# Kernel tuning notes

Measured on AMD Instinct MI355X. Metric: run time of the kernel, lower is better.

Reference implementation:

```python
import jax, jax.numpy as jnp
import numpy as np

N, E, F_IN, H, C, G, NC = 50000, 800000, 128, 4, 64, 512, 10
NEG_SLOPE = 0.2


def setup_inputs() -> dict:
    key = jax.random.key(0)
    ks = jax.random.split(key, 16)
    s = lambda fan: 1.0 / np.sqrt(fan)
    inp = {
        'x': jax.random.normal(ks[0], (N, F_IN), jnp.float32),
        'edge_index': jax.random.randint(ks[1], (2, E), 0, N, jnp.int64),
        'batch': jnp.sort(jax.random.randint(ks[2], (N,), 0, G, jnp.int64)),
        # conv1: F_IN -> H*C, concat
        'W1': jax.random.normal(ks[3], (F_IN, H * C), jnp.float32) * s(F_IN),
        'a_src1': jax.random.normal(ks[4], (H, C), jnp.float32) * s(C),
        'a_dst1': jax.random.normal(ks[5], (H, C), jnp.float32) * s(C),
        'b1': jnp.zeros((H * C,), jnp.float32),
        # conv2: H*C -> H*C, concat
        'W2': jax.random.normal(ks[6], (H * C, H * C), jnp.float32) * s(H * C),
        'a_src2': jax.random.normal(ks[7], (H, C), jnp.float32) * s(C),
        'a_dst2': jax.random.normal(ks[8], (H, C), jnp.float32) * s(C),
        'b2': jnp.zeros((H * C,), jnp.float32),
        # conv3: H*C -> C, concat=False (mean over heads)
        'W3': jax.random.normal(ks[9], (H * C, H * C), jnp.float32) * s(H * C),
        'a_src3': jax.random.normal(ks[10], (H, C), jnp.float32) * s(C),
        'a_dst3': jax.random.normal(ks[11], (H, C), jnp.float32) * s(C),
        'b3': jnp.zeros((C,), jnp.float32),
        # final linear: C -> NC
        'Wl': jax.random.normal(ks[12], (C, NC), jnp.float32) * s(C),
        'bl': jnp.zeros((NC,), jnp.float32),
    }
    return inp


def _gat_conv(x, src, dst, W, a_src, a_dst, b, concat):
    n = x.shape[0]
    h = (x @ W).reshape(n, H, C)                       # [N,H,C]
    al_src = jnp.sum(h * a_src, axis=-1)               # [N,H]
    al_dst = jnp.sum(h * a_dst, axis=-1)               # [N,H]
    e = al_src[src] + al_dst[dst]                      # [E',H] per-edge logits
    e = jax.nn.leaky_relu(e, NEG_SLOPE)
    # segment softmax over incoming edges of each dst node
    m = jax.ops.segment_max(e, dst, num_segments=n)
    ex = jnp.exp(e - m[dst])
    z = jax.ops.segment_sum(ex, dst, num_segments=n)
    alpha = ex / (z[dst] + 1e-16)                      # [E',H]
    msg = h[src] * alpha[:, :, None]                   # [E',H,C]
    out = jax.ops.segment_sum(msg, dst, num_segments=n)  # [N,H,C]
    out = out.reshape(n, H * C) if concat else out.mean(axis=1)
    return out + b


def reference(x, edge_index, batch, W1, a_src1, a_dst1, b1, W2, a_src2, a_dst2, b2,
              W3, a_src3, a_dst3, b3, Wl, bl):
    n = x.shape[0]
    loops = jnp.arange(n, dtype=edge_index.dtype)
    src = jnp.concatenate([edge_index[0], loops])      # add self-loops (PyG default)
    dst = jnp.concatenate([edge_index[1], loops])
    h = jax.nn.relu(_gat_conv(x, src, dst, W1, a_src1, a_dst1, b1, True))
    h = jax.nn.relu(_gat_conv(h, src, dst, W2, a_src2, a_dst2, b2, True))
    h = jax.nn.relu(_gat_conv(h, src, dst, W3, a_src3, a_dst3, b3, False))
    # global mean pool over graphs
    sums = jax.ops.segment_sum(h, batch, num_segments=G)          # [G,C]
    cnts = jax.ops.segment_sum(jnp.ones((n,), h.dtype), batch, num_segments=G)
    pooled = sums / jnp.maximum(cnts, 1.0)[:, None]
    # dropout is identity in eval mode
    return pooled @ Wl + bl                                       # [G,NC]
```

## Files before the change

kernel.cpp:

```cpp
#include <hip/hip_runtime.h>

#define N_NODES 50000
#define E_EDGES 800000
#define E_TOT   (E_EDGES + N_NODES)
#define F_INDIM 128
#define NHEAD   4
#define CDIM    64
#define HC      256
#define NGRAPH  512
#define NCLS    10
#define NEG_SLOPE 0.2f
#define AGG_BLOCKS 2048
#define NP (N_NODES + 128)
#define XCHUNKS (N_NODES * F_INDIM / 8)

typedef __attribute__((ext_vector_type(8))) _Float16 f16x8;
typedef __attribute__((ext_vector_type(8))) unsigned short ushort8;
typedef __attribute__((ext_vector_type(4))) float f32x4;

__device__ inline float leakyf(float x) { return x > 0.f ? x : NEG_SLOPE * x; }
__device__ inline unsigned short f2h(float x) {
  _Float16 h = (_Float16)x;
  return __builtin_bit_cast(unsigned short, h);
}
__device__ inline float h2f(unsigned short u) {
  return (float)__builtin_bit_cast(_Float16, u);
}

#define GLL16(gp, lp) \
  __builtin_amdgcn_global_load_lds((const __attribute__((address_space(1))) void*)(gp), \
                                   (__attribute__((address_space(3))) void*)(lp), 16, 0, 0)

__global__ __launch_bounds__(256) void k_hist(const int* __restrict__ ei, int* __restrict__ deg) {
  int e = blockIdx.x * 256 + threadIdx.x;
  if (e < E_EDGES) atomicAdd(&deg[ei[E_EDGES + e]], 1);
}

__global__ __launch_bounds__(256) void k_scan1(const int* __restrict__ deg, int* __restrict__ incl,
                                               int* __restrict__ blksum) {
  __shared__ int s[256];
  int tid = threadIdx.x;
  int i = blockIdx.x * 256 + tid;
  int v = (i < N_NODES) ? (deg[i] + 1) : 0;
  s[tid] = v;
  __syncthreads();
  for (int d = 1; d < 256; d <<= 1) {
    int t = (tid >= d) ? s[tid - d] : 0;
    __syncthreads();
    s[tid] += t;
    __syncthreads();
  }
  if (i < N_NODES) incl[i] = s[tid];
  if (tid == 255) blksum[blockIdx.x] = s[255];
}

__global__ __launch_bounds__(256) void k_scan2(int* __restrict__ blksum, int nblk) {
  __shared__ int s[256];
  int tid = threadIdx.x;
  int v = (tid < nblk) ? blksum[tid] : 0;
  s[tid] = v;
  __syncthreads();
  for (int d = 1; d < 256; d <<= 1) {
    int t = (tid >= d) ? s[tid - d] : 0;
    __syncthreads();
    s[tid] += t;
    __syncthreads();
  }
  if (tid < nblk) blksum[tid] = s[tid] - v;
}

__global__ __launch_bounds__(256) void k_scan3(const int* __restrict__ deg, int* __restrict__ off,
                                               const int* __restrict__ blksum, int* __restrict__ cursor) {
  int i = blockIdx.x * 256 + threadIdx.x;
  if (i < N_NODES) {
    int excl = off[i] - (deg[i] + 1) + blksum[blockIdx.x];
    off[i] = excl;
    cursor[i] = excl;
  }
  if (i == 0) off[N_NODES] = E_TOT;
}

__global__ __launch_bounds__(256) void k_fill(const int* __restrict__ ei, int* __restrict__ cursor,
                                              int* __restrict__ csr_src) {
  int idx = blockIdx.x * 256 + threadIdx.x;
  if (idx >= E_TOT) return;
  int s, d;
  if (idx < E_EDGES) { s = ei[idx]; d = ei[E_EDGES + idx]; }
  else               { s = idx - E_EDGES; d = s; }
  int pos = atomicAdd(&cursor[d], 1);
  csr_src[pos] = s;
}

__global__ __launch_bounds__(256) void k_cvt_all(const float* __restrict__ x,
                                                 const float* __restrict__ W1,
                                                 const float* __restrict__ W2,
                                                 const float* __restrict__ W3,
                                                 unsigned short* __restrict__ xh,
                                                 unsigned short* __restrict__ Wt1,
                                                 unsigned short* __restrict__ Wt2,
                                                 unsigned short* __restrict__ Wt3) {
  int i = blockIdx.x * 256 + threadIdx.x;
  if (i < XCHUNKS) {
    float4 v0 = *(const float4*)&x[(size_t)i * 8];
    float4 v1 = *(const float4*)&x[(size_t)i * 8 + 4];
    ushort8 o;
    o[0] = f2h(v0.x); o[1] = f2h(v0.y); o[2] = f2h(v0.z); o[3] = f2h(v0.w);
    o[4] = f2h(v1.x); o[5] = f2h(v1.y); o[6] = f2h(v1.z); o[7] = f2h(v1.w);
    *(ushort8*)&xh[(size_t)i * 8] = o;
    return;
  }
  int j = i - XCHUNKS;
  if (j < F_INDIM * HC) {
    int k = j >> 8, n = j & 255;
    Wt1[n * F_INDIM + k] = f2h(W1[j]);
    return;
  }
  j -= F_INDIM * HC;
  if (j < HC * HC) {
    int k = j >> 8, n = j & 255;
    Wt2[n * HC + k] = f2h(W2[j]);
    return;
  }
  j -= HC * HC;
  if (j < HC * HC) {
    int k = j >> 8, n = j & 255;
    Wt3[n * HC + k] = f2h(W3[j]);
  }
}

template<int K, bool ASL>
__global__ __launch_bounds__(256) void k_gemm_f16(const unsigned short* __restrict__ A,
                                                  const unsigned short* __restrict__ Bt,
                                                  unsigned short* __restrict__ C,
                                                  const float* __restrict__ a_src,
                                                  const float* __restrict__ a_dst,
                                                  float* __restrict__ al_s,
                                                  float* __restrict__ al_d) {
  __shared__ unsigned short As[128 * 64];
  __shared__ unsigned short Bs[128 * 64];
  int tid = threadIdx.x;
  int w = tid >> 6, l = tid & 63;
  int wm = w >> 1, wn = w & 1;
  int m0 = blockIdx.x * 128, n0 = blockIdx.y * 128;
  int fl = l & 15, qq = l >> 4;
  int w32 = w * 32;
  int l3 = l >> 3;
  int csw = (l & 7) ^ (l3 & 7);
  f32x4 acc[4][4] = {};

  for (int k0 = 0; k0 < K; k0 += 64) {
    int kc = k0 + csw * 8;
#pragma unroll
    for (int j = 0; j < 4; ++j) {
      int r = w32 + j * 8 + l3;
      const unsigned short* ap;
      if (ASL) ap = &A[(size_t)(kc >> 7) * NP * 128 + (size_t)(m0 + r) * 128 + (kc & 127)];
      else     ap = &A[(size_t)(m0 + r) * K + kc];
      GLL16(ap, &As[(w32 + j * 8) * 64]);
      GLL16(&Bt[(size_t)(n0 + r) * K + kc], &Bs[(w32 + j * 8) * 64]);
    }
    __syncthreads();
#pragma unroll
    for (int kk = 0; kk < 2; ++kk) {
      f16x8 af[4], bf[4];
      int sl = ((kk * 4 + qq) ^ (fl & 7)) * 8;
#pragma unroll
      for (int f = 0; f < 4; ++f) {
        af[f] = *(const f16x8*)&As[(wm * 64 + f * 16 + fl) * 64 + sl];
        bf[f] = *(const f16x8*)&Bs[(wn * 64 + f * 16 + fl) * 64 + sl];
      }
#pragma unroll
      for (int f = 0; f < 4; ++f)
#pragma unroll
        for (int g = 0; g < 4; ++g)
          acc[f][g] = __builtin_amdgcn_mfma_f32_16x16x32_f16(af[f], bf[g], acc[f][g], 0, 0, 0);
    }
    if (k0 + 64 < K) __syncthreads();
  }

  int cr = qq * 4;
  unsigned short* Cs = C + (size_t)blockIdx.y * NP * 128;
#pragma unroll
  for (int f = 0; f < 4; ++f) {
    int mrow = m0 + wm * 64 + f * 16 + cr;
#pragma unroll
    for (int r = 0; r < 4; ++r) {
      if (mrow + r < N_NODES) {
#pragma unroll
        for (int g = 0; g < 4; ++g)
          Cs[(size_t)(mrow + r) * 128 + wn * 64 + g * 16 + fl] = f2h(acc[f][g][r]);
      }
    }
  }
  int head = blockIdx.y * 2 + wn;
  float as_r[4], ad_r[4];
#pragma unroll
  for (int g = 0; g < 4; ++g) {
    as_r[g] = a_src[head * 64 + g * 16 + fl];
    ad_r[g] = a_dst[head * 64 + g * 16 + fl];
  }
#pragma unroll
  for (int f = 0; f < 4; ++f) {
#pragma unroll
    for (int r = 0; r < 4; ++r) {
      float ps = 0.f, pd = 0.f;
#pragma unroll
      for (int g = 0; g < 4; ++g) {
        ps = fmaf(as_r[g], acc[f][g][r], ps);
        pd = fmaf(ad_r[g], acc[f][g][r], pd);
      }
#pragma unroll
      for (int o = 1; o < 16; o <<= 1) { ps += __shfl_xor(ps, o); pd += __shfl_xor(pd, o); }
      if (fl == 0) {
        int row = m0 + wm * 64 + f * 16 + cr + r;
        if (row < N_NODES) {
          al_s[row * 4 + head] = ps;
          al_d[row * 4 + head] = pd;
        }
      }
    }
  }
}

template<bool CONCAT>
__global__ __launch_bounds__(256) void k_aggregate(
    const unsigned short* __restrict__ h_sl, const int* __restrict__ off,
    const int* __restrict__ csr_src,
    const float* __restrict__ al_s, const float* __restrict__ al_d,
    const float* __restrict__ bias, unsigned short* __restrict__ out_sl,
    float* __restrict__ out_pf) {
  __shared__ float s_p[4][64][4];
  __shared__ int   s_src[4][64];
  int tid = threadIdx.x;
  int wv = tid >> 6;
  int lane = tid & 63;
  int grp = lane >> 4;
  int cl = lane & 15;
  int cg = cl << 3;
  int slice = blockIdx.x & 1;
  int head = slice * 2 + (cl >> 3);
  const unsigned short* __restrict__ hs = h_sl + (size_t)slice * NP * 128;
  float bv[8];
  if (CONCAT) {
#pragma unroll
    for (int i = 0; i < 8; ++i) bv[i] = bias[slice * 128 + cg + i];
  }

  const int STRIDE = (AGG_BLOCKS / 2) * 4;
  for (int d = (blockIdx.x >> 1) * 4 + wv; d < N_NODES; d += STRIDE) {
    int lo  = off[d];
    int deg = off[d + 1] - lo;
    float4 adv = *(const float4*)&al_d[(size_t)d * 4];

    float z0 = 0.f, z1 = 0.f, z2 = 0.f, z3 = 0.f;
    for (int e = lane; e < deg; e += 64) {
      int s = csr_src[lo + e];
      float4 asv = *(const float4*)&al_s[(size_t)s * 4];
      float p0 = __expf(leakyf(asv.x + adv.x));
      float p1 = __expf(leakyf(asv.y + adv.y));
      float p2 = __expf(leakyf(asv.z + adv.z));
      float p3 = __expf(leakyf(asv.w + adv.w));
      if (e < 64) {
        s_p[wv][e][0] = p0; s_p[wv][e][1] = p1;
        s_p[wv][e][2] = p2; s_p[wv][e][3] = p3;
        s_src[wv][e] = s;
      }
      z0 += p0; z1 += p1; z2 += p2; z3 += p3;
    }
#pragma unroll
    for (int o = 1; o < 64; o <<= 1) {
      z0 += __shfl_xor(z0, o); z1 += __shfl_xor(z1, o);
      z2 += __shfl_xor(z2, o); z3 += __shfl_xor(z3, o);
    }
    float zih = 1.f / ((head == 0 ? z0 : (head == 1 ? z1 : (head == 2 ? z2 : z3))) + 1e-16f);

    int dcap = min(deg, 64);
    float acc[8] = {};
    int e = grp;
    for (; e + 12 < dcap; e += 16) {
      int sv[4]; float pv[4]; ushort8 hv[4];
#pragma unroll
      for (int q = 0; q < 4; ++q) {
        int ee = e + q * 4;
        sv[q] = s_src[wv][ee];
        pv[q] = s_p[wv][ee][head];
      }
#pragma unroll
      for (int q = 0; q < 4; ++q) hv[q] = *(const ushort8*)&hs[(size_t)sv[q] * 128 + cg];
#pragma unroll
      for (int q = 0; q < 4; ++q)
#pragma unroll
        for (int i = 0; i < 8; ++i) acc[i] = fmaf(pv[q], h2f(hv[q][i]), acc[i]);
    }
    for (; e < dcap; e += 4) {
      int s = s_src[wv][e];
      float p = s_p[wv][e][head];
      ushort8 hv = *(const ushort8*)&hs[(size_t)s * 128 + cg];
#pragma unroll
      for (int i = 0; i < 8; ++i) acc[i] = fmaf(p, h2f(hv[i]), acc[i]);
    }
    if (deg > 64) {
      for (int e2 = 64 + grp; e2 < deg; e2 += 4) {
        int s = csr_src[lo + e2];
        float4 asv = *(const float4*)&al_s[(size_t)s * 4];
        float q0 = __expf(leakyf(asv.x + adv.x));
        float q1 = __expf(leakyf(asv.y + adv.y));
        float q2 = __expf(leakyf(asv.z + adv.z));
        float q3 = __expf(leakyf(asv.w + adv.w));
        float p = head == 0 ? q0 : (head == 1 ? q1 : (head == 2 ? q2 : q3));
        ushort8 hv = *(const ushort8*)&hs[(size_t)s * 128 + cg];
#pragma unroll
        for (int i = 0; i < 8; ++i) acc[i] = fmaf(p, h2f(hv[i]), acc[i]);
      }
    }

#pragma unroll
    for (int i = 0; i < 8; ++i) {
      acc[i] += __shfl_xor(acc[i], 16);
      acc[i] += __shfl_xor(acc[i], 32);
      acc[i] *= zih;
    }

    if (CONCAT) {
      if (lane < 16) {
        ushort8 o;
#pragma unroll
        for (int i = 0; i < 8; ++i) o[i] = f2h(fmaxf(acc[i] + bv[i], 0.f));
        *(ushort8*)&out_sl[(size_t)slice * NP * 128 + (size_t)d * 128 + cg] = o;
      }
    } else {
#pragma unroll
      for (int i = 0; i < 8; ++i) acc[i] += __shfl_xor(acc[i], 8);
      if (lane < 8) {
        float* pf = &out_pf[(size_t)slice * N_NODES * CDIM + (size_t)d * CDIM + cg];
        *(float4*)&pf[0] = make_float4(acc[0], acc[1], acc[2], acc[3]);
        *(float4*)&pf[4] = make_float4(acc[4], acc[5], acc[6], acc[7]);
      }
    }
  }
}

__device__ inline int lower_bound_i(const int* __restrict__ a, int n, int key) {
  int lo = 0, hi = n;
  while (lo < hi) { int mid = (lo + hi) >> 1; if (a[mid] < key) lo = mid + 1; else hi = mid; }
  return lo;
}

__global__ __launch_bounds__(256) void k_pool(const float* __restrict__ pf,
                                              const int* __restrict__ batch,
                                              const float* __restrict__ b3,
                                              const float* __restrict__ Wl, const float* __restrict__ bl,
                                              float* __restrict__ out) {
  int g = blockIdx.x, tid = threadIdx.x;
  int lo = lower_bound_i(batch, N_NODES, g);
  int hi = lower_bound_i(batch, N_NODES, g + 1);
  int c = tid & 63, sl = tid >> 6;
  float bc = b3[c];
  float acc = 0.f;
  for (int n = lo + sl; n < hi; n += 4) {
    float v = pf[(size_t)n * CDIM + c] + pf[(size_t)N_NODES * CDIM + (size_t)n * CDIM + c];
    acc += fmaxf(0.25f * v + bc, 0.f);
  }
  __shared__ float s[256];
  __shared__ float pooled[64];
  s[tid] = acc;
  __syncthreads();
  if (tid < 64) {
    float cnt = fmaxf((float)(hi - lo), 1.f);
    pooled[tid] = (s[tid] + s[tid + 64] + s[tid + 128] + s[tid + 192]) / cnt;
  }
  __syncthreads();
  if (tid < NCLS) {
    float o = bl[tid];
    for (int cc = 0; cc < CDIM; ++cc)
      o = fmaf(pooled[cc], Wl[cc * NCLS + tid], o);
    out[g * NCLS + tid] = o;
  }
}

extern "C" void kernel_launch(void* const* d_in, const int* in_sizes, int n_in,
                              void* d_out, int out_size, void* d_ws, size_t ws_size,
                              hipStream_t stream) {
  const float* x     = (const float*)d_in[0];
  const int*   ei    = (const int*)d_in[1];
  const int*   batch = (const int*)d_in[2];
  const float* W1  = (const float*)d_in[3];
  const float* as1 = (const float*)d_in[4];
  const float* ad1 = (const float*)d_in[5];
  const float* b1  = (const float*)d_in[6];
  const float* W2  = (const float*)d_in[7];
  const float* as2 = (const float*)d_in[8];
  const float* ad2 = (const float*)d_in[9];
  const float* b2  = (const float*)d_in[10];
  const float* W3  = (const float*)d_in[11];
  const float* as3 = (const float*)d_in[12];
  const float* ad3 = (const float*)d_in[13];
  const float* b3  = (const float*)d_in[14];
  const float* Wl  = (const float*)d_in[15];
  const float* bl  = (const float*)d_in[16];
  float* out = (float*)d_out;

  char* ws = (char*)d_ws;
  size_t o = 0;
  auto alloc = [&](size_t bytes) -> void* {
    void* p = ws + o;
    o += (bytes + 255) & ~(size_t)255;
    return p;
  };
  unsigned short* hbuf  = (unsigned short*)alloc((size_t)2 * NP * 128 * 2);
  unsigned short* abuf  = (unsigned short*)alloc((size_t)2 * NP * 128 * 2);
  unsigned short* x_h   = (unsigned short*)alloc((size_t)NP * F_INDIM * 2);
  unsigned short* Wt1   = (unsigned short*)alloc((size_t)HC * F_INDIM * 2);
  unsigned short* Wt2   = (unsigned short*)alloc((size_t)HC * HC * 2);
  unsigned short* Wt3   = (unsigned short*)alloc((size_t)HC * HC * 2);
  float* al_s  = (float*)alloc((size_t)N_NODES * 4 * 4);
  float* al_d  = (float*)alloc((size_t)N_NODES * 4 * 4);
  float* pf    = (float*)alloc((size_t)2 * N_NODES * CDIM * 4);
  int*   deg   = (int*)alloc((size_t)N_NODES * 4);
  int*   off   = (int*)alloc((size_t)(N_NODES + 1) * 4);
  int*   cursor= (int*)alloc((size_t)N_NODES * 4);
  int*   blksum= (int*)alloc(1024);
  int*   csr   = (int*)alloc((size_t)E_TOT * 4);

  int nblk = (N_NODES + 255) / 256;
  hipMemsetAsync(deg, 0, (size_t)N_NODES * 4, stream);
  k_hist<<<(E_EDGES + 255) / 256, 256, 0, stream>>>(ei, deg);
  k_scan1<<<nblk, 256, 0, stream>>>(deg, off, blksum);
  k_scan2<<<1, 256, 0, stream>>>(blksum, nblk);
  k_scan3<<<nblk, 256, 0, stream>>>(deg, off, blksum, cursor);
  k_fill<<<(E_TOT + 255) / 256, 256, 0, stream>>>(ei, cursor, csr);

  int cvt_total = XCHUNKS + F_INDIM * HC + 2 * HC * HC;
  k_cvt_all<<<(cvt_total + 255) / 256, 256, 0, stream>>>(x, W1, W2, W3, x_h, Wt1, Wt2, Wt3);

  dim3 ggrid((N_NODES + 127) / 128, HC / 128);
  k_gemm_f16<F_INDIM, false><<<ggrid, 256, 0, stream>>>(x_h, Wt1, hbuf, as1, ad1, al_s, al_d);
  k_aggregate<true><<<AGG_BLOCKS, 256, 0, stream>>>(hbuf, off, csr, al_s, al_d, b1, abuf, nullptr);
  k_gemm_f16<HC, true><<<ggrid, 256, 0, stream>>>(abuf, Wt2, hbuf, as2, ad2, al_s, al_d);
  k_aggregate<true><<<AGG_BLOCKS, 256, 0, stream>>>(hbuf, off, csr, al_s, al_d, b2, abuf, nullptr);
  k_gemm_f16<HC, true><<<ggrid, 256, 0, stream>>>(abuf, Wt3, hbuf, as3, ad3, al_s, al_d);
  k_aggregate<false><<<AGG_BLOCKS, 256, 0, stream>>>(hbuf, off, csr, al_s, al_d, b3, nullptr, pf);
  k_pool<<<NGRAPH, 256, 0, stream>>>(pf, batch, b3, Wl, bl, out);
}
```

Measured before the change: 449.2 us.

## Slice node features per head so each aggregate block gathers one head

```diff
diff --git a/kernel.cpp b/kernel.cpp
--- a/kernel.cpp
+++ b/kernel.cpp
@@ -154,7 +154,7 @@
     for (int j = 0; j < 4; ++j) {
       int r = w32 + j * 8 + l3;
       const unsigned short* ap;
-      if (ASL) ap = &A[(size_t)(kc >> 7) * NP * 128 + (size_t)(m0 + r) * 128 + (kc & 127)];
+      if (ASL) ap = &A[(size_t)(kc >> 6) * NP * 64 + (size_t)(m0 + r) * 64 + (kc & 63)];
       else     ap = &A[(size_t)(m0 + r) * K + kc];
       GLL16(ap, &As[(w32 + j * 8) * 64]);
       GLL16(&Bt[(size_t)(n0 + r) * K + kc], &Bs[(w32 + j * 8) * 64]);
@@ -179,7 +179,8 @@
   }
 
   int cr = qq * 4;
-  unsigned short* Cs = C + (size_t)blockIdx.y * NP * 128;
+  int head = blockIdx.y * 2 + wn;
+  unsigned short* Cs = C + (size_t)head * NP * 64;
 #pragma unroll
   for (int f = 0; f < 4; ++f) {
     int mrow = m0 + wm * 64 + f * 16 + cr;
@@ -188,11 +189,10 @@
       if (mrow + r < N_NODES) {
 #pragma unroll
         for (int g = 0; g < 4; ++g)
-          Cs[(size_t)(mrow + r) * 128 + wn * 64 + g * 16 + fl] = f2h(acc[f][g][r]);
-      }
-    }
-  }
-  int head = blockIdx.y * 2 + wn;
+          Cs[(size_t)(mrow + r) * 64 + g * 16 + fl] = f2h(acc[f][g][r]);
+      }
+    }
+  }
   float as_r[4], ad_r[4];
 #pragma unroll
   for (int g = 0; g < 4; ++g) {
@@ -228,87 +228,70 @@
     const int* __restrict__ csr_src,
     const float* __restrict__ al_s, const float* __restrict__ al_d,
     const float* __restrict__ bias, unsigned short* __restrict__ out_sl,
-    float* __restrict__ out_pf) {
-  __shared__ float s_p[4][64][4];
+    unsigned short* __restrict__ out_pf) {
+  __shared__ float s_p[4][64];
   __shared__ int   s_src[4][64];
   int tid = threadIdx.x;
   int wv = tid >> 6;
   int lane = tid & 63;
-  int grp = lane >> 4;
-  int cl = lane & 15;
+  int grp = lane >> 3;
+  int cl = lane & 7;
   int cg = cl << 3;
-  int slice = blockIdx.x & 1;
-  int head = slice * 2 + (cl >> 3);
-  const unsigned short* __restrict__ hs = h_sl + (size_t)slice * NP * 128;
+  int slice = blockIdx.x & 3;
+  const unsigned short* __restrict__ hs = h_sl + (size_t)slice * NP * 64;
   float bv[8];
   if (CONCAT) {
 #pragma unroll
-    for (int i = 0; i < 8; ++i) bv[i] = bias[slice * 128 + cg + i];
-  }
-
-  const int STRIDE = (AGG_BLOCKS / 2) * 4;
-  for (int d = (blockIdx.x >> 1) * 4 + wv; d < N_NODES; d += STRIDE) {
+    for (int i = 0; i < 8; ++i) bv[i] = bias[slice * 64 + cg + i];
+  }
+
+  const int STRIDE = (AGG_BLOCKS / 4) * 4;
+  for (int d = (blockIdx.x >> 2) * 4 + wv; d < N_NODES; d += STRIDE) {
     int lo  = off[d];
     int deg = off[d + 1] - lo;
-    float4 adv = *(const float4*)&al_d[(size_t)d * 4];
-
-    float z0 = 0.f, z1 = 0.f, z2 = 0.f, z3 = 0.f;
+    float ad = al_d[(size_t)d * 4 + slice];
+
+    float z = 0.f;
     for (int e = lane; e < deg; e += 64) {
       int s = csr_src[lo + e];
-      float4 asv = *(const float4*)&al_s[(size_t)s * 4];
-      float p0 = __expf(leakyf(asv.x + adv.x));
-      float p1 = __expf(leakyf(asv.y + adv.y));
-      float p2 = __expf(leakyf(asv.z + adv.z));
-      float p3 = __expf(leakyf(asv.w + adv.w));
-      if (e < 64) {
-        s_p[wv][e][0] = p0; s_p[wv][e][1] = p1;
-        s_p[wv][e][2] = p2; s_p[wv][e][3] = p3;
-        s_src[wv][e] = s;
-      }
-      z0 += p0; z1 += p1; z2 += p2; z3 += p3;
-    }
-#pragma unroll
-    for (int o = 1; o < 64; o <<= 1) {
-      z0 += __shfl_xor(z0, o); z1 += __shfl_xor(z1, o);
-      z2 += __shfl_xor(z2, o); z3 += __shfl_xor(z3, o);
-    }
-    float zih = 1.f / ((head == 0 ? z0 : (head == 1 ? z1 : (head == 2 ? z2 : z3))) + 1e-16f);
+      float p = __expf(leakyf(al_s[(size_t)s * 4 + slice] + ad));
+      if (e < 64) { s_p[wv][e] = p; s_src[wv][e] = s; }
+      z += p;
+    }
+#pragma unroll
+    for (int o = 1; o < 64; o <<= 1) z += __shfl_xor(z, o);
+    float zih = 1.f / (z + 1e-16f);
 
     int dcap = min(deg, 64);
     float acc[8] = {};
     int e = grp;
-    for (; e + 12 < dcap; e += 16) {
+    for (; e + 24 < dcap; e += 32) {
       int sv[4]; float pv[4]; ushort8 hv[4];
 #pragma unroll
       for (int q = 0; q < 4; ++q) {
-        int ee = e + q * 4;
+        int ee = e + q * 8;
         sv[q] = s_src[wv][ee];
-        pv[q] = s_p[wv][ee][head];
-      }
-#pragma unroll
-      for (int q = 0; q < 4; ++q) hv[q] = *(const ushort8*)&hs[(size_t)sv[q] * 128 + cg];
+        pv[q] = s_p[wv][ee];
+      }
+#pragma unroll
+      for (int q = 0; q < 4; ++q) hv[q] = *(const ushort8*)&hs[(size_t)sv[q] * 64 + cg];
 #pragma unroll
       for (int q = 0; q < 4; ++q)
 #pragma unroll
         for (int i = 0; i < 8; ++i) acc[i] = fmaf(pv[q], h2f(hv[q][i]), acc[i]);
     }
-    for (; e < dcap; e += 4) {
+    for (; e < dcap; e += 8) {
       int s = s_src[wv][e];
-      float p = s_p[wv][e][head];
-      ushort8 hv = *(const ushort8*)&hs[(size_t)s * 128 + cg];
+      float p = s_p[wv][e];
+      ushort8 hv = *(const ushort8*)&hs[(size_t)s * 64 + cg];
 #pragma unroll
       for (int i = 0; i < 8; ++i) acc[i] = fmaf(p, h2f(hv[i]), acc[i]);
     }
     if (deg > 64) {
-      for (int e2 = 64 + grp; e2 < deg; e2 += 4) {
+      for (int e2 = 64 + grp; e2 < deg; e2 += 8) {
         int s = csr_src[lo + e2];
-        float4 asv = *(const float4*)&al_s[(size_t)s * 4];
-        float q0 = __expf(leakyf(asv.x + adv.x));
-        float q1 = __expf(leakyf(asv.y + adv.y));
-        float q2 = __expf(leakyf(asv.z + adv.z));
-        float q3 = __expf(leakyf(asv.w + adv.w));
-        float p = head == 0 ? q0 : (head == 1 ? q1 : (head == 2 ? q2 : q3));
-        ushort8 hv = *(const ushort8*)&hs[(size_t)s * 128 + cg];
+        float p = __expf(leakyf(al_s[(size_t)s * 4 + slice] + ad));
+        ushort8 hv = *(const ushort8*)&hs[(size_t)s * 64 + cg];
 #pragma unroll
         for (int i = 0; i < 8; ++i) acc[i] = fmaf(p, h2f(hv[i]), acc[i]);
       }
@@ -316,25 +299,22 @@
 
 #pragma unroll
     for (int i = 0; i < 8; ++i) {
+      acc[i] += __shfl_xor(acc[i], 8);
       acc[i] += __shfl_xor(acc[i], 16);
       acc[i] += __shfl_xor(acc[i], 32);
       acc[i] *= zih;
     }
 
-    if (CONCAT) {
-      if (lane < 16) {
-        ushort8 o;
+    if (lane < 8) {
+      ushort8 o;
+      if (CONCAT) {
 #pragma unroll
         for (int i = 0; i < 8; ++i) o[i] = f2h(fmaxf(acc[i] + bv[i], 0.f));
-        *(ushort8*)&out_sl[(size_t)slice * NP * 128 + (size_t)d * 128 + cg] = o;
-      }
-    } else {
-#pragma unroll
-      for (int i = 0; i < 8; ++i) acc[i] += __shfl_xor(acc[i], 8);
-      if (lane < 8) {
-        float* pf = &out_pf[(size_t)slice * N_NODES * CDIM + (size_t)d * CDIM + cg];
-        *(float4*)&pf[0] = make_float4(acc[0], acc[1], acc[2], acc[3]);
-        *(float4*)&pf[4] = make_float4(acc[4], acc[5], acc[6], acc[7]);
+        *(ushort8*)&out_sl[(size_t)slice * NP * 64 + (size_t)d * 64 + cg] = o;
+      } else {
+#pragma unroll
+        for (int i = 0; i < 8; ++i) o[i] = f2h(acc[i]);
+        *(ushort8*)&out_pf[(size_t)slice * N_NODES * 64 + (size_t)d * 64 + cg] = o;
       }
     }
   }
@@ -346,7 +326,7 @@
   return lo;
 }
 
-__global__ __launch_bounds__(256) void k_pool(const float* __restrict__ pf,
+__global__ __launch_bounds__(256) void k_pool(const unsigned short* __restrict__ pf,
                                               const int* __restrict__ batch,
                                               const float* __restrict__ b3,
                                               const float* __restrict__ Wl, const float* __restrict__ bl,
@@ -358,7 +338,10 @@
   float bc = b3[c];
   float acc = 0.f;
   for (int n = lo + sl; n < hi; n += 4) {
-    float v = pf[(size_t)n * CDIM + c] + pf[(size_t)N_NODES * CDIM + (size_t)n * CDIM + c];
+    float v = h2f(pf[(size_t)0 * N_NODES * 64 + (size_t)n * 64 + c])
+            + h2f(pf[(size_t)1 * N_NODES * 64 + (size_t)n * 64 + c])
+            + h2f(pf[(size_t)2 * N_NODES * 64 + (size_t)n * 64 + c])
+            + h2f(pf[(size_t)3 * N_NODES * 64 + (size_t)n * 64 + c]);
     acc += fmaxf(0.25f * v + bc, 0.f);
   }
   __shared__ float s[256];
@@ -407,15 +390,15 @@
     o += (bytes + 255) & ~(size_t)255;
     return p;
   };
-  unsigned short* hbuf  = (unsigned short*)alloc((size_t)2 * NP * 128 * 2);
-  unsigned short* abuf  = (unsigned short*)alloc((size_t)2 * NP * 128 * 2);
+  unsigned short* hbuf  = (unsigned short*)alloc((size_t)4 * NP * 64 * 2);
+  unsigned short* abuf  = (unsigned short*)alloc((size_t)4 * NP * 64 * 2);
+  unsigned short* pf    = (unsigned short*)alloc((size_t)4 * N_NODES * 64 * 2);
   unsigned short* x_h   = (unsigned short*)alloc((size_t)NP * F_INDIM * 2);
   unsigned short* Wt1   = (unsigned short*)alloc((size_t)HC * F_INDIM * 2);
   unsigned short* Wt2   = (unsigned short*)alloc((size_t)HC * HC * 2);
   unsigned short* Wt3   = (unsigned short*)alloc((size_t)HC * HC * 2);
   float* al_s  = (float*)alloc((size_t)N_NODES * 4 * 4);
   float* al_d  = (float*)alloc((size_t)N_NODES * 4 * 4);
-  float* pf    = (float*)alloc((size_t)2 * N_NODES * CDIM * 4);
   int*   deg   = (int*)alloc((size_t)N_NODES * 4);
   int*   off   = (int*)alloc((size_t)(N_NODES + 1) * 4);
   int*   cursor= (int*)alloc((size_t)N_NODES * 4);
```

After: 579.3 us. 1.29x slower.
